# Performance work log

Hardware: AMD Instinct MI355X
Metric: run time of the kernel (lower is better)

The kernel has to match this reference:

```python
import jax, jax.numpy as jnp
import numpy as np

N_NODES = 50000
N_EDGES = 800000
N_GRAPHS = 64
NEG_SLOPE = 0.2


def _gat_layer(x, src, dst, W, a_src, a_dst, b, heads, out_ch):
    """PyG-style GATConv (concat=True, eval mode, self loops already in src/dst)."""
    N = x.shape[0]
    h = (x @ W).reshape(N, heads, out_ch)                 # [N,H,C]
    al_src = jnp.sum(h * a_src, axis=-1)                  # [N,H]
    al_dst = jnp.sum(h * a_dst, axis=-1)                  # [N,H]
    e = jax.nn.leaky_relu(al_src[src] + al_dst[dst], NEG_SLOPE)  # [E,H]
    m = jax.ops.segment_max(e, dst, num_segments=N)       # scatter-softmax (stable)
    e = jnp.exp(e - m[dst])
    s = jax.ops.segment_sum(e, dst, num_segments=N)
    alpha = e / (s[dst] + 1e-16)                          # [E,H]
    msg = h[src] * alpha[..., None]                       # [E,H,C]
    out = jax.ops.segment_sum(msg, dst, num_segments=N)   # [N,H,C]
    return out.reshape(N, heads * out_ch) + b


def setup_inputs() -> dict:
    key = jax.random.key(0)
    ks = jax.random.split(key, 20)
    x = jax.random.normal(ks[0], (N_NODES, 2), dtype=jnp.float32)
    edge_index = jax.random.randint(ks[1], (2, N_EDGES), 0, N_NODES, dtype=jnp.int64)
    batch = jnp.sort(jax.random.randint(ks[2], (N_NODES,), 0, N_GRAPHS, dtype=jnp.int64))

    def glorot(k, shape):
        fan = sum(shape)
        return jax.random.uniform(k, shape, jnp.float32, -1.0, 1.0) * jnp.sqrt(6.0 / fan)

    return {
        "x": x, "edge_index": edge_index, "batch": batch,
        # gat1: 2 -> 64, heads=2, concat -> 128
        "w1": glorot(ks[3], (2, 128)),
        "a_src1": glorot(ks[4], (2, 64)),
        "a_dst1": glorot(ks[5], (2, 64)),
        "b1": jnp.zeros((128,), jnp.float32),
        # gat2: 128 -> 64, heads=1
        "w2": glorot(ks[6], (128, 64)),
        "a_src2": glorot(ks[7], (1, 64)),
        "a_dst2": glorot(ks[8], (1, 64)),
        "b2": jnp.zeros((64,), jnp.float32),
        # gat3: 64 -> 64, heads=1
        "w3": glorot(ks[9], (64, 64)),
        "a_src3": glorot(ks[10], (1, 64)),
        "a_dst3": glorot(ks[11], (1, 64)),
        "b3": jnp.zeros((64,), jnp.float32),
        # MLP head
        "fw1": glorot(ks[12], (64, 32)),
        "fb1": jnp.zeros((32,), jnp.float32),
        "fw2": glorot(ks[13], (32, 1)),
        "fb2": jnp.zeros((1,), jnp.float32),
    }


def reference(x, edge_index, batch,
              w1, a_src1, a_dst1, b1,
              w2, a_src2, a_dst2, b2,
              w3, a_src3, a_dst3, b3,
              fw1, fb1, fw2, fb2):
    N = x.shape[0]
    loops = jnp.arange(N, dtype=edge_index.dtype)
    src = jnp.concatenate([edge_index[0], loops])  # add self loops (PyG default)
    dst = jnp.concatenate([edge_index[1], loops])

    h = jax.nn.elu(_gat_layer(x, src, dst, w1, a_src1, a_dst1, b1, heads=2, out_ch=64))
    h = jax.nn.elu(_gat_layer(h, src, dst, w2, a_src2, a_dst2, b2, heads=1, out_ch=64))
    h = jax.nn.elu(_gat_layer(h, src, dst, w3, a_src3, a_dst3, b3, heads=1, out_ch=64))

    # global mean pool
    sums = jax.ops.segment_sum(h, batch, num_segments=N_GRAPHS)          # [B,64]
    cnts = jax.ops.segment_sum(jnp.ones((N,), h.dtype), batch, num_segments=N_GRAPHS)
    g = sums / jnp.maximum(cnts, 1.0)[:, None]

    g = jax.nn.relu(g @ fw1 + fb1)
    return g @ fw2 + fb2
```

## Files before the change

kernel.cpp:

```cpp
#include <hip/hip_runtime.h>
#include <hip/hip_bf16.h>
#include <math.h>

#define NN 50000
#define NE 800000
#define ET 850000
#define NG 64

#define NBUK 125
#define BS   400
#define CHK  8192
#define NCH  104
#define NHIST (NBUK * NCH)
#define NSB  ((NHIST + 255) / 256)


__global__ __launch_bounds__(256) void hist_k(const int* __restrict__ ei,
                                              int* __restrict__ ghist) {
    __shared__ int h[NBUK];
    int c = blockIdx.x, t = threadIdx.x;
    for (int i = t; i < NBUK; i += 256) h[i] = 0;
    __syncthreads();
    int e0 = c * CHK;
    int e1 = min(ET, e0 + CHK);
    for (int e = e0 + t; e < e1; e += 256) {
        int dst = (e < NE) ? ei[NE + e] : (e - NE);
        atomicAdd(&h[dst / BS], 1);
    }
    __syncthreads();
    for (int b = t; b < NBUK; b += 256) ghist[b * NCH + c] = h[b];
}

__global__ __launch_bounds__(256) void gscan1_k(const int* __restrict__ in,
                                                int* __restrict__ out,
                                                int* __restrict__ bsum, int n) {
    int t = threadIdx.x;
    int idx = blockIdx.x * 256 + t;
    int v = (idx < n) ? in[idx] : 0;
    int lane = t & 63, wave = t >> 6;
    int inc = v;
#pragma unroll
    for (int d = 1; d < 64; d <<= 1) {
        int u = __shfl_up(inc, d);
        if (lane >= d) inc += u;
    }
    __shared__ int wtot[4];
    if (lane == 63) wtot[wave] = inc;
    __syncthreads();
    int wpre = 0;
    for (int w = 0; w < wave; w++) wpre += wtot[w];
    if (idx < n) out[idx] = wpre + inc - v;
    if (t == 255) bsum[blockIdx.x] = wpre + inc;
}

__global__ __launch_bounds__(256) void gscan2_k(const int* __restrict__ bsum,
                                                int* __restrict__ bpre, int nb,
                                                int* __restrict__ tailp, int tailv) {
    int t = threadIdx.x;
    int v = (t < nb) ? bsum[t] : 0;
    int lane = t & 63, wave = t >> 6;
    int inc = v;
#pragma unroll
    for (int d = 1; d < 64; d <<= 1) {
        int u = __shfl_up(inc, d);
        if (lane >= d) inc += u;
    }
    __shared__ int wtot[4];
    if (lane == 63) wtot[wave] = inc;
    __syncthreads();
    int wpre = 0;
    for (int w = 0; w < wave; w++) wpre += wtot[w];
    if (t < nb) bpre[t] = wpre + inc - v;
    if (t == 0 && tailp) *tailp = tailv;
}

__global__ __launch_bounds__(256) void gscan3_k(int* __restrict__ out,
                                                const int* __restrict__ bpre, int n) {
    int idx = blockIdx.x * 256 + threadIdx.x;
    if (idx < n) out[idx] += bpre[blockIdx.x];
}

__global__ __launch_bounds__(256) void part_k(const int* __restrict__ ei,
                                              const int* __restrict__ gbase,
                                              int* __restrict__ packed) {
    __shared__ int cur[NBUK];
    __shared__ int baseL[NBUK];
    int c = blockIdx.x, t = threadIdx.x;
    for (int i = t; i < NBUK; i += 256) {
        cur[i] = 0;
        baseL[i] = gbase[i * NCH + c];
    }
    __syncthreads();
    int e0 = c * CHK;
    int e1 = min(ET, e0 + CHK);
    for (int e = e0 + t; e < e1; e += 256) {
        int src, dst;
        if (e < NE) { src = ei[e]; dst = ei[NE + e]; }
        else        { src = dst = e - NE; }
        int b = dst / BS;
        int r = atomicAdd(&cur[b], 1);
        packed[baseL[b] + r] = ((dst - b * BS) << 17) | src;
    }
}

__global__ __launch_bounds__(256) void csr_k(const int* __restrict__ packed,
                                             const int* __restrict__ gbase,
                                             int* __restrict__ csr,
                                             int* __restrict__ offsets) {
    __shared__ int cnt[BS];
    __shared__ int sc[2][512];
    __shared__ int cur[BS];
    __shared__ int Ss, Ts;
    int b = blockIdx.x, t = threadIdx.x;
    for (int i = t; i < BS; i += 256) cnt[i] = 0;
    if (t == 0) {
        Ss = gbase[b * NCH];
        Ts = (b == NBUK - 1) ? ET : gbase[(b + 1) * NCH];
    }
    __syncthreads();
    int n0 = Ss, n1 = Ts;
    for (int i = n0 + t; i < n1; i += 256) {
        int p = packed[i];
        atomicAdd(&cnt[p >> 17], 1);
    }
    __syncthreads();
    for (int i = t; i < 512; i += 256) sc[0][i] = (i < BS) ? cnt[i] : 0;
    __syncthreads();
    int pp = 0;
    for (int d = 1; d < 512; d <<= 1) {
        for (int i = t; i < 512; i += 256) {
            int v = sc[pp][i];
            if (i >= d) v += sc[pp][i - d];
            sc[pp ^ 1][i] = v;
        }
        pp ^= 1;
        __syncthreads();
    }
    for (int i = t; i < BS; i += 256) {
        int pre = (i == 0) ? 0 : sc[pp][i - 1];
        offsets[b * BS + i] = Ss + pre;
        cur[i] = Ss + pre;
    }
    __syncthreads();
    for (int i = n0 + t; i < n1; i += 256) {
        int p = packed[i];
        int pos = atomicAdd(&cur[p >> 17], 1);
        csr[pos] = p & 0x1FFFF;
    }
}

__global__ __launch_bounds__(256) void sortw_k(const int* __restrict__ offsets,
                                               int* __restrict__ csr) {
    int gt = blockIdx.x * blockDim.x + threadIdx.x;
    int n = gt >> 6;
    int lane = gt & 63;
    if (n >= NN) return;
    int b0 = offsets[n], b1 = offsets[n + 1];
    int deg = b1 - b0;
    if (deg <= 1) return;
    if (deg <= 64) {
        int v = (lane < deg) ? csr[b0 + lane] : 0x7FFFFFFF;
#pragma unroll
        for (int k = 2; k <= 64; k <<= 1) {
#pragma unroll
            for (int j = k >> 1; j > 0; j >>= 1) {
                int partner = __shfl_xor(v, j);
                bool up = ((lane & k) == 0);
                bool keepmin = (((lane & j) == 0) == up);
                v = keepmin ? min(v, partner) : max(v, partner);
            }
        }
        if (lane < deg) csr[b0 + lane] = v;
    } else if (lane == 0) {
        for (int i = b0 + 1; i < b1; i++) {
            int v = csr[i];
            int j = i - 1;
            while (j >= b0 && csr[j] > v) { csr[j + 1] = csr[j]; j--; }
            csr[j + 1] = v;
        }
    }
}


__global__ __launch_bounds__(256) void feat1b_k(const float* __restrict__ x,
                                                const float* __restrict__ w1,
                                                const float* __restrict__ as1,
                                                const float* __restrict__ ad1,
                                                float* __restrict__ alS,
                                                float* __restrict__ alD) {
    int t = threadIdx.x;
    int tt = t & 127;
    int n = blockIdx.x * 2 + (t >> 7);
    float x0 = x[n * 2 + 0], x1 = x[n * 2 + 1];
    float v = x0 * w1[tt] + x1 * w1[128 + tt];
    int head = (t >> 6) & 1, lane = t & 63;
    float ps = v * as1[tt];
    float pd = v * ad1[tt];
    for (int d = 32; d; d >>= 1) {
        ps += __shfl_down(ps, d);
        pd += __shfl_down(pd, d);
    }
    if (lane == 0) {
        alS[n * 2 + head] = ps;
        alD[n * 2 + head] = pd;
    }
}


__global__ __launch_bounds__(256) void agg1_k(const float2* __restrict__ x2,
                                              const float* __restrict__ w1,
                                              const float* __restrict__ alS,
                                              const float* __restrict__ alD,
                                              const float* __restrict__ bias,
                                              const int* __restrict__ offsets,
                                              const int* __restrict__ csr,
                                              float* __restrict__ out) {
    __shared__ float4 wslds[4][64];
    int t = threadIdx.x;
    int wave = t >> 6, lane = t & 63, grp = lane >> 4, c4 = lane & 15;
    int gl = lane & 15;
    int n = blockIdx.x * 4 + wave;
    int b0 = offsets[n], b1 = offsets[n + 1];
    int deg = b1 - b0;
    float2 adv = ((const float2*)alD)[n];
    const float2* alS2 = (const float2*)alS;

    float4 wa0 = ((const float4*)w1)[c4];
    float4 wa1 = ((const float4*)w1)[16 + c4];
    float4 wb0 = ((const float4*)(w1 + 128))[c4];
    float4 wb1 = ((const float4*)(w1 + 128))[16 + c4];
    float4 acc0 = make_float4(0.f, 0.f, 0.f, 0.f);
    float4 acc1 = make_float4(0.f, 0.f, 0.f, 0.f);
    float inv0, inv1;

    if (deg <= 64) {
        bool valid = lane < deg;
        int s = 0; float ev0 = -1e30f, ev1 = -1e30f;
        float2 xs = make_float2(0.f, 0.f);
        if (valid) {
            s = csr[b0 + lane];
            float2 al = alS2[s];
            xs = x2[s];
            float e0 = al.x + adv.x;
            ev0 = e0 > 0.f ? e0 : 0.2f * e0;
            float e1 = al.y + adv.y;
            ev1 = e1 > 0.f ? e1 : 0.2f * e1;
        }
        float m0 = ev0, m1 = ev1;
#pragma unroll
        for (int d = 32; d; d >>= 1) {
            m0 = fmaxf(m0, __shfl_xor(m0, d));
            m1 = fmaxf(m1, __shfl_xor(m1, d));
        }
        if (valid) {
            float w0 = expf(ev0 - m0);
            float w1v = expf(ev1 - m1);
            wslds[wave][lane] = make_float4(w0, w1v, xs.x, xs.y);
        }
        float ssum0 = 0.f, ssum1 = 0.f;
#pragma unroll
        for (int k = 0; k < 4; k++) {
            int j = gl + 16 * k;
            if (j < deg) {
                float4 f = wslds[wave][j];
                ssum0 += f.x;
                ssum1 += f.y;
            }
        }
        for (int d = 8; d; d >>= 1) {
            ssum0 += __shfl_xor(ssum0, d);
            ssum1 += __shfl_xor(ssum1, d);
        }
        inv0 = 1.f / (ssum0 + 1e-16f);
        inv1 = 1.f / (ssum1 + 1e-16f);
        int j = grp;
        for (; j + 12 < deg; j += 16) {
            float4 f0 = wslds[wave][j];
            float4 f1 = wslds[wave][j + 4];
            float4 f2 = wslds[wave][j + 8];
            float4 f3 = wslds[wave][j + 12];
            float4 v;
            v.x = f0.z * wa0.x + f0.w * wb0.x;
            v.y = f0.z * wa0.y + f0.w * wb0.y;
            v.z = f0.z * wa0.z + f0.w * wb0.z;
            v.w = f0.z * wa0.w + f0.w * wb0.w;
            acc0.x = fmaf(f0.x, v.x, acc0.x);
            acc0.y = fmaf(f0.x, v.y, acc0.y);
            acc0.z = fmaf(f0.x, v.z, acc0.z);
            acc0.w = fmaf(f0.x, v.w, acc0.w);
            v.x = f0.z * wa1.x + f0.w * wb1.x;
            v.y = f0.z * wa1.y + f0.w * wb1.y;
            v.z = f0.z * wa1.z + f0.w * wb1.z;
            v.w = f0.z * wa1.w + f0.w * wb1.w;
            acc1.x = fmaf(f0.y, v.x, acc1.x);
            acc1.y = fmaf(f0.y, v.y, acc1.y);
            acc1.z = fmaf(f0.y, v.z, acc1.z);
            acc1.w = fmaf(f0.y, v.w, acc1.w);
            v.x = f1.z * wa0.x + f1.w * wb0.x;
            v.y = f1.z * wa0.y + f1.w * wb0.y;
            v.z = f1.z * wa0.z + f1.w * wb0.z;
            v.w = f1.z * wa0.w + f1.w * wb0.w;
            acc0.x = fmaf(f1.x, v.x, acc0.x);
            acc0.y = fmaf(f1.x, v.y, acc0.y);
            acc0.z = fmaf(f1.x, v.z, acc0.z);
            acc0.w = fmaf(f1.x, v.w, acc0.w);
            v.x = f1.z * wa1.x + f1.w * wb1.x;
            v.y = f1.z * wa1.y + f1.w * wb1.y;
            v.z = f1.z * wa1.z + f1.w * wb1.z;
            v.w = f1.z * wa1.w + f1.w * wb1.w;
            acc1.x = fmaf(f1.y, v.x, acc1.x);
            acc1.y = fmaf(f1.y, v.y, acc1.y);
            acc1.z = fmaf(f1.y, v.z, acc1.z);
            acc1.w = fmaf(f1.y, v.w, acc1.w);
            v.x = f2.z * wa0.x + f2.w * wb0.x;
            v.y = f2.z * wa0.y + f2.w * wb0.y;
            v.z = f2.z * wa0.z + f2.w * wb0.z;
            v.w = f2.z * wa0.w + f2.w * wb0.w;
            acc0.x = fmaf(f2.x, v.x, acc0.x);
            acc0.y = fmaf(f2.x, v.y, acc0.y);
            acc0.z = fmaf(f2.x, v.z, acc0.z);
            acc0.w = fmaf(f2.x, v.w, acc0.w);
            v.x = f2.z * wa1.x + f2.w * wb1.x;
            v.y = f2.z * wa1.y + f2.w * wb1.y;
            v.z = f2.z * wa1.z + f2.w * wb1.z;
            v.w = f2.z * wa1.w + f2.w * wb1.w;
            acc1.x = fmaf(f2.y, v.x, acc1.x);
            acc1.y = fmaf(f2.y, v.y, acc1.y);
            acc1.z = fmaf(f2.y, v.z, acc1.z);
            acc1.w = fmaf(f2.y, v.w, acc1.w);
            v.x = f3.z * wa0.x + f3.w * wb0.x;
            v.y = f3.z * wa0.y + f3.w * wb0.y;
            v.z = f3.z * wa0.z + f3.w * wb0.z;
            v.w = f3.z * wa0.w + f3.w * wb0.w;
            acc0.x = fmaf(f3.x, v.x, acc0.x);
            acc0.y = fmaf(f3.x, v.y, acc0.y);
            acc0.z = fmaf(f3.x, v.z, acc0.z);
            acc0.w = fmaf(f3.x, v.w, acc0.w);
            v.x = f3.z * wa1.x + f3.w * wb1.x;
            v.y = f3.z * wa1.y + f3.w * wb1.y;
            v.z = f3.z * wa1.z + f3.w * wb1.z;
            v.w = f3.z * wa1.w + f3.w * wb1.w;
            acc1.x = fmaf(f3.y, v.x, acc1.x);
            acc1.y = fmaf(f3.y, v.y, acc1.y);
            acc1.z = fmaf(f3.y, v.z, acc1.z);
            acc1.w = fmaf(f3.y, v.w, acc1.w);
        }
        for (; j < deg; j += 4) {
            float4 f0 = wslds[wave][j];
            float4 v;
            v.x = f0.z * wa0.x + f0.w * wb0.x;
            v.y = f0.z * wa0.y + f0.w * wb0.y;
            v.z = f0.z * wa0.z + f0.w * wb0.z;
            v.w = f0.z * wa0.w + f0.w * wb0.w;
            acc0.x = fmaf(f0.x, v.x, acc0.x);
            acc0.y = fmaf(f0.x, v.y, acc0.y);
            acc0.z = fmaf(f0.x, v.z, acc0.z);
            acc0.w = fmaf(f0.x, v.w, acc0.w);
            v.x = f0.z * wa1.x + f0.w * wb1.x;
            v.y = f0.z * wa1.y + f0.w * wb1.y;
            v.z = f0.z * wa1.z + f0.w * wb1.z;
            v.w = f0.z * wa1.w + f0.w * wb1.w;
            acc1.x = fmaf(f0.y, v.x, acc1.x);
            acc1.y = fmaf(f0.y, v.y, acc1.y);
            acc1.z = fmaf(f0.y, v.z, acc1.z);
            acc1.w = fmaf(f0.y, v.w, acc1.w);
        }
    } else {
        for (int head = 0; head < 2; head++) {
            float ad = head ? adv.y : adv.x;
            float4 wa = head ? wa1 : wa0, wb = head ? wb1 : wb0;
            float m = -1e30f;
            for (int i = b0 + gl; i < b1; i += 16) {
                int s = csr[i];
                float ev = alS[s * 2 + head] + ad;
                ev = ev > 0.f ? ev : 0.2f * ev;
                m = fmaxf(m, ev);
            }
            for (int d = 8; d; d >>= 1) m = fmaxf(m, __shfl_xor(m, d));
            float ssum = 0.f;
            for (int i = b0 + gl; i < b1; i += 16) {
                int s = csr[i];
                float ev = alS[s * 2 + head] + ad;
                ev = ev > 0.f ? ev : 0.2f * ev;
                float w = expf(ev - m);
                ssum += w;
            }
            for (int d = 8; d; d >>= 1) ssum += __shfl_xor(ssum, d);
            float invh = 1.f / (ssum + 1e-16f);
            float4 acc = make_float4(0.f, 0.f, 0.f, 0.f);
            for (int i = b0 + grp; i < b1; i += 4) {
                int s = csr[i];
                float ev = alS[s * 2 + head] + ad;
                ev = ev > 0.f ? ev : 0.2f * ev;
                float w = expf(ev - m);
                float2 xs = x2[s];
                float4 v;
                v.x = xs.x * wa.x + xs.y * wb.x;
                v.y = xs.x * wa.y + xs.y * wb.y;
                v.z = xs.x * wa.z + xs.y * wb.z;
                v.w = xs.x * wa.w + xs.y * wb.w;
                acc.x = fmaf(w, v.x, acc.x);
                acc.y = fmaf(w, v.y, acc.y);
                acc.z = fmaf(w, v.z, acc.z);
                acc.w = fmaf(w, v.w, acc.w);
            }
            if (head == 0) { acc0 = acc; inv0 = invh; }
            else           { acc1 = acc; inv1 = invh; }
        }
    }
#pragma unroll
    for (int mask = 16; mask <= 32; mask <<= 1) {
        acc0.x += __shfl_xor(acc0.x, mask);
        acc0.y += __shfl_xor(acc0.y, mask);
        acc0.z += __shfl_xor(acc0.z, mask);
        acc0.w += __shfl_xor(acc0.w, mask);
        acc1.x += __shfl_xor(acc1.x, mask);
        acc1.y += __shfl_xor(acc1.y, mask);
        acc1.z += __shfl_xor(acc1.z, mask);
        acc1.w += __shfl_xor(acc1.w, mask);
    }
    if (grp < 2) {
        float4 acc = (grp == 0) ? acc0 : acc1;
        float inv = (grp == 0) ? inv0 : inv1;
        float4 b = ((const float4*)bias)[grp * 16 + c4];
        float4 r;
        r.x = acc.x * inv + b.x;
        r.y = acc.y * inv + b.y;
        r.z = acc.z * inv + b.z;
        r.w = acc.w * inv + b.w;
        r.x = r.x > 0.f ? r.x : expm1f(r.x);
        r.y = r.y > 0.f ? r.y : expm1f(r.y);
        r.z = r.z > 0.f ? r.z : expm1f(r.z);
        r.w = r.w > 0.f ? r.w : expm1f(r.w);
        ((float4*)out)[((size_t)n * 2 + grp) * 16 + c4] = r;
    }
}


template <int K>
__global__ __launch_bounds__(256) void gemm_al_k(const float* __restrict__ in,
                                                 const float* __restrict__ W,
                                                 const float* __restrict__ as,
                                                 const float* __restrict__ ad,
                                                 float* __restrict__ h,
                                                 float* __restrict__ alS,
                                                 float* __restrict__ alD) {
    __shared__ float Wl[K * 64];
    __shared__ float rowb[16][K];
    int t = threadIdx.x;
    for (int i = t; i < K * 64; i += 256) Wl[i] = W[i];
    int wave = t >> 6, c = t & 63;
    int nb = blockIdx.x * 16 + wave * 4;
#pragma unroll
    for (int r = 0; r < 4; r++) {
        const float* row = in + (size_t)(nb + r) * K;
        for (int k = c; k < K; k += 64) rowb[wave * 4 + r][k] = row[k];
    }
    __syncthreads();
    const float* rb0 = rowb[wave * 4 + 0];
    const float* rb1 = rowb[wave * 4 + 1];
    const float* rb2 = rowb[wave * 4 + 2];
    const float* rb3 = rowb[wave * 4 + 3];
    float a0 = 0.f, a1 = 0.f, a2 = 0.f, a3 = 0.f;
#pragma unroll 4
    for (int k = 0; k < K; k++) {
        float wv = Wl[k * 64 + c];
        a0 = fmaf(rb0[k], wv, a0);
        a1 = fmaf(rb1[k], wv, a1);
        a2 = fmaf(rb2[k], wv, a2);
        a3 = fmaf(rb3[k], wv, a3);
    }
    h[(size_t)(nb + 0) * 64 + c] = a0;
    h[(size_t)(nb + 1) * 64 + c] = a1;
    h[(size_t)(nb + 2) * 64 + c] = a2;
    h[(size_t)(nb + 3) * 64 + c] = a3;
    float asc = as[c], adc = ad[c];
    float ps0 = a0 * asc, pd0 = a0 * adc;
    float ps1 = a1 * asc, pd1 = a1 * adc;
    float ps2 = a2 * asc, pd2 = a2 * adc;
    float ps3 = a3 * asc, pd3 = a3 * adc;
    for (int d = 32; d; d >>= 1) {
        ps0 += __shfl_down(ps0, d); pd0 += __shfl_down(pd0, d);
        ps1 += __shfl_down(ps1, d); pd1 += __shfl_down(pd1, d);
        ps2 += __shfl_down(ps2, d); pd2 += __shfl_down(pd2, d);
        ps3 += __shfl_down(ps3, d); pd3 += __shfl_down(pd3, d);
    }
    if (c == 0) {
        alS[nb + 0] = ps0; alD[nb + 0] = pd0;
        alS[nb + 1] = ps1; alD[nb + 1] = pd1;
        alS[nb + 2] = ps2; alD[nb + 2] = pd2;
        alS[nb + 3] = ps3; alD[nb + 3] = pd3;
    }
}


__global__ __launch_bounds__(256) void aggf2_k(const float4* __restrict__ h4,
                                               const float* __restrict__ alS,
                                               const float* __restrict__ alD,
                                               const float* __restrict__ bias,
                                               const int* __restrict__ offsets,
                                               const int* __restrict__ csr,
                                               float* __restrict__ out) {
    __shared__ float2 wlds[4][64];
    int t = threadIdx.x;
    int wave = t >> 6, lane = t & 63, grp = lane >> 4, c4 = lane & 15;
    int gl = lane & 15;
    int n = blockIdx.x * 4 + wave;
    int b0 = offsets[n], b1 = offsets[n + 1];
    int deg = b1 - b0;
    float adn = alD[n];

    float4 acc = make_float4(0.f, 0.f, 0.f, 0.f);
    float inv;

    if (deg <= 64) {
        bool valid = lane < deg;
        int s = 0; float ev = -1e30f;
        if (valid) {
            s = csr[b0 + lane];
            float e0 = alS[s] + adn;
            ev = e0 > 0.f ? e0 : 0.2f * e0;
        }
        float m = ev;
#pragma unroll
        for (int d = 32; d; d >>= 1) m = fmaxf(m, __shfl_xor(m, d));
        if (valid) {
            float w = expf(ev - m);
            wlds[wave][lane] = make_float2(w, __int_as_float(s));
        }
        float ssum = 0.f;
#pragma unroll
        for (int k = 0; k < 4; k++) {
            int j = gl + 16 * k;
            if (j < deg) ssum += wlds[wave][j].x;
        }
        for (int d = 8; d; d >>= 1) ssum += __shfl_xor(ssum, d);
        inv = 1.f / (ssum + 1e-16f);
        int j = grp;
        for (; j + 12 < deg; j += 16) {
            float2 f0 = wlds[wave][j];
            float2 f1 = wlds[wave][j + 4];
            float2 f2 = wlds[wave][j + 8];
            float2 f3 = wlds[wave][j + 12];
            float4 v0 = h4[(size_t)__float_as_int(f0.y) * 16 + c4];
            float4 v1 = h4[(size_t)__float_as_int(f1.y) * 16 + c4];
            float4 v2 = h4[(size_t)__float_as_int(f2.y) * 16 + c4];
            float4 v3 = h4[(size_t)__float_as_int(f3.y) * 16 + c4];
            acc.x = fmaf(f0.x, v0.x, acc.x);
            acc.y = fmaf(f0.x, v0.y, acc.y);
            acc.z = fmaf(f0.x, v0.z, acc.z);
            acc.w = fmaf(f0.x, v0.w, acc.w);
            acc.x = fmaf(f1.x, v1.x, acc.x);
            acc.y = fmaf(f1.x, v1.y, acc.y);
            acc.z = fmaf(f1.x, v1.z, acc.z);
            acc.w = fmaf(f1.x, v1.w, acc.w);
            acc.x = fmaf(f2.x, v2.x, acc.x);
            acc.y = fmaf(f2.x, v2.y, acc.y);
            acc.z = fmaf(f2.x, v2.z, acc.z);
            acc.w = fmaf(f2.x, v2.w, acc.w);
            acc.x = fmaf(f3.x, v3.x, acc.x);
            acc.y = fmaf(f3.x, v3.y, acc.y);
            acc.z = fmaf(f3.x, v3.z, acc.z);
            acc.w = fmaf(f3.x, v3.w, acc.w);
        }
        for (; j < deg; j += 4) {
            float2 f0 = wlds[wave][j];
            float4 v0 = h4[(size_t)__float_as_int(f0.y) * 16 + c4];
            acc.x = fmaf(f0.x, v0.x, acc.x);
            acc.y = fmaf(f0.x, v0.y, acc.y);
            acc.z = fmaf(f0.x, v0.z, acc.z);
            acc.w = fmaf(f0.x, v0.w, acc.w);
        }
    } else {
        float m = -1e30f;
        for (int i = b0 + gl; i < b1; i += 16) {
            int s = csr[i];
            float ev = alS[s] + adn;
            ev = ev > 0.f ? ev : 0.2f * ev;
            m = fmaxf(m, ev);
        }
        for (int d = 8; d; d >>= 1) m = fmaxf(m, __shfl_xor(m, d));
        float ssum = 0.f;
        for (int i = b0 + gl; i < b1; i += 16) {
            int s = csr[i];
            float ev = alS[s] + adn;
            ev = ev > 0.f ? ev : 0.2f * ev;
            float w = expf(ev - m);
            ssum += w;
        }
        for (int d = 8; d; d >>= 1) ssum += __shfl_xor(ssum, d);
        inv = 1.f / (ssum + 1e-16f);
        for (int i = b0 + grp; i < b1; i += 4) {
            int s = csr[i];
            float ev = alS[s] + adn;
            ev = ev > 0.f ? ev : 0.2f * ev;
            float w = expf(ev - m);
            float4 v = h4[(size_t)s * 16 + c4];
            acc.x = fmaf(w, v.x, acc.x);
            acc.y = fmaf(w, v.y, acc.y);
            acc.z = fmaf(w, v.z, acc.z);
            acc.w = fmaf(w, v.w, acc.w);
        }
    }
#pragma unroll
    for (int mask = 16; mask <= 32; mask <<= 1) {
        acc.x += __shfl_xor(acc.x, mask);
        acc.y += __shfl_xor(acc.y, mask);
        acc.z += __shfl_xor(acc.z, mask);
        acc.w += __shfl_xor(acc.w, mask);
    }
    if (grp == 0) {
        float4 b = ((const float4*)bias)[c4];
        float4 r;
        r.x = acc.x * inv + b.x;
        r.y = acc.y * inv + b.y;
        r.z = acc.z * inv + b.z;
        r.w = acc.w * inv + b.w;
        r.x = r.x > 0.f ? r.x : expm1f(r.x);
        r.y = r.y > 0.f ? r.y : expm1f(r.y);
        r.z = r.z > 0.f ? r.z : expm1f(r.z);
        r.w = r.w > 0.f ? r.w : expm1f(r.w);
        ((float4*)out)[(size_t)n * 16 + c4] = r;
    }
}


__global__ __launch_bounds__(1024) void pool_k(const float* __restrict__ h,
                                               const int* __restrict__ batch,
                                               float* __restrict__ gout) {
    int g = blockIdx.x;
    __shared__ int sb, se;
    __shared__ float partial[16][64];
    int t = threadIdx.x, wave = t >> 6, c = t & 63;
    if (t == 0) {
        int lo = 0, hi = NN;
        while (lo < hi) { int mid = (lo + hi) >> 1; if (batch[mid] < g) lo = mid + 1; else hi = mid; }
        sb = lo;
        lo = 0; hi = NN;
        while (lo < hi) { int mid = (lo + hi) >> 1; if (batch[mid] < g + 1) lo = mid + 1; else hi = mid; }
        se = lo;
    }
    __syncthreads();
    float acc = 0.f;
    for (int r = sb + wave; r < se; r += 16) acc += h[(size_t)r * 64 + c];
    partial[wave][c] = acc;
    __syncthreads();
    if (wave == 0) {
        float s = 0.f;
#pragma unroll
        for (int wv = 0; wv < 16; wv++) s += partial[wv][c];
        int cnt = se - sb;
        gout[g * 64 + c] = s / fmaxf((float)cnt, 1.0f);
    }
}


__global__ __launch_bounds__(64) void mlp_k(const float* __restrict__ g,
                                            const float* __restrict__ fw1,
                                            const float* __restrict__ fb1,
                                            const float* __restrict__ fw2,
                                            const float* __restrict__ fb2,
                                            float* __restrict__ out) {
    int gi = blockIdx.x;
    __shared__ float gv[64];
    __shared__ float hid[32];
    int t = threadIdx.x;
    gv[t] = g[gi * 64 + t];
    __syncthreads();
    if (t < 32) {
        float a = fb1[t];
        for (int c = 0; c < 64; c++) a += gv[c] * fw1[c * 32 + t];
        hid[t] = a > 0.f ? a : 0.f;
    }
    __syncthreads();
    if (t == 0) {
        float o = fb2[0];
        for (int j = 0; j < 32; j++) o += hid[j] * fw2[j];
        out[gi] = o;
    }
}


extern "C" void kernel_launch(void* const* d_in, const int* in_sizes, int n_in,
                              void* d_out, int out_size, void* d_ws, size_t ws_size,
                              hipStream_t stream) {
    const float* x   = (const float*)d_in[0];
    const int*   ei  = (const int*)d_in[1];
    const int*   bat = (const int*)d_in[2];
    const float* w1  = (const float*)d_in[3];
    const float* as1 = (const float*)d_in[4];
    const float* ad1 = (const float*)d_in[5];
    const float* b1  = (const float*)d_in[6];
    const float* w2  = (const float*)d_in[7];
    const float* as2 = (const float*)d_in[8];
    const float* ad2 = (const float*)d_in[9];
    const float* b2  = (const float*)d_in[10];
    const float* w3  = (const float*)d_in[11];
    const float* as3 = (const float*)d_in[12];
    const float* ad3 = (const float*)d_in[13];
    const float* b3  = (const float*)d_in[14];
    const float* fw1 = (const float*)d_in[15];
    const float* fb1 = (const float*)d_in[16];
    const float* fw2 = (const float*)d_in[17];
    const float* fb2 = (const float*)d_in[18];
    float* out = (float*)d_out;

    char* ws = (char*)d_ws;
    size_t o = 0;
    auto alloc = [&](size_t bytes) -> void* {
        void* p = ws + o;
        o += (bytes + 255) & ~(size_t)255;
        return p;
    };
    int*    offsets = (int*)alloc((NN + 1) * sizeof(int));
    int*    ghist   = (int*)alloc(NHIST * sizeof(int));
    int*    gbase   = (int*)alloc(NHIST * sizeof(int));
    int*    bsum    = (int*)alloc(NSB * sizeof(int));
    int*    bpre    = (int*)alloc(NSB * sizeof(int));
    int*    packed  = (int*)alloc(ET * sizeof(int));
    int*    csr     = (int*)alloc(ET * sizeof(int));
    float*  l1out   = (float*)alloc((size_t)NN * 128 * sizeof(float));
    float*  hX      = (float*)alloc((size_t)NN * 64 * sizeof(float));
    float*  l2out   = (float*)alloc((size_t)NN * 64 * sizeof(float));
    float*  l3out   = (float*)alloc((size_t)NN * 64 * sizeof(float));
    float*  alS     = (float*)alloc((size_t)NN * 2 * sizeof(float));
    float*  alD     = (float*)alloc((size_t)NN * 2 * sizeof(float));
    float*  gbuf    = (float*)alloc((size_t)NG * 64 * sizeof(float));

    hist_k<<<NCH, 256, 0, stream>>>(ei, ghist);
    gscan1_k<<<NSB, 256, 0, stream>>>(ghist, gbase, bsum, NHIST);
    gscan2_k<<<1, 256, 0, stream>>>(bsum, bpre, NSB, offsets + NN, ET);
    gscan3_k<<<NSB, 256, 0, stream>>>(gbase, bpre, NHIST);
    part_k<<<NCH, 256, 0, stream>>>(ei, gbase, packed);
    csr_k<<<NBUK, 256, 0, stream>>>(packed, gbase, csr, offsets);
    sortw_k<<<NN / 4, 256, 0, stream>>>(offsets, csr);

    feat1b_k<<<NN / 2, 256, 0, stream>>>(x, w1, as1, ad1, alS, alD);
    agg1_k<<<NN / 4, 256, 0, stream>>>((const float2*)x, w1, alS, alD, b1, offsets, csr, l1out);

    gemm_al_k<128><<<NN / 16, 256, 0, stream>>>(l1out, w2, as2, ad2, hX, alS, alD);
    aggf2_k<<<NN / 4, 256, 0, stream>>>((const float4*)hX, alS, alD, b2, offsets, csr, l2out);

    gemm_al_k<64><<<NN / 16, 256, 0, stream>>>(l2out, w3, as3, ad3, hX, alS, alD);
    aggf2_k<<<NN / 4, 256, 0, stream>>>((const float4*)hX, alS, alD, b3, offsets, csr, l3out);

    pool_k<<<NG, 1024, 0, stream>>>(l3out, bat, gbuf);
    mlp_k<<<NG, 64, 0, stream>>>(gbuf, fw1, fb1, fw2, fb2, out);
}
```

Measured before the change: 281.9 us.

## Process four nodes per wave in aggregation kernels and fold scan fixup into consumers

The aggregation kernels now give each wave four destination nodes instead of one. When all four degrees are at most 64, their gathers, softmax reductions and shuffles are interleaved so more memory requests are in flight at once and weight and bias loads are shared; otherwise they fall back to a per-node helper. Separately, the gscan3 fixup kernel is removed and its block prefix is added on the fly in part_k and csr_k, saving one launch and one pass over the histogram. The interleaved path raises register and LDS use per wave, which may lower occupancy, and the grid shrinks to a quarter as many blocks.

Result: no change. 285.1 us (+1.1%).

```diff
diff --git a/kernel.cpp b/kernel.cpp
--- a/kernel.cpp
+++ b/kernel.cpp
@@ -74,21 +74,17 @@
     if (t == 0 && tailp) *tailp = tailv;
 }
 
-__global__ __launch_bounds__(256) void gscan3_k(int* __restrict__ out,
-                                                const int* __restrict__ bpre, int n) {
-    int idx = blockIdx.x * 256 + threadIdx.x;
-    if (idx < n) out[idx] += bpre[blockIdx.x];
-}
-
 __global__ __launch_bounds__(256) void part_k(const int* __restrict__ ei,
                                               const int* __restrict__ gbase,
+                                              const int* __restrict__ bpre,
                                               int* __restrict__ packed) {
     __shared__ int cur[NBUK];
     __shared__ int baseL[NBUK];
     int c = blockIdx.x, t = threadIdx.x;
     for (int i = t; i < NBUK; i += 256) {
+        int idx = i * NCH + c;
         cur[i] = 0;
-        baseL[i] = gbase[i * NCH + c];
+        baseL[i] = gbase[idx] + bpre[idx >> 8];
     }
     __syncthreads();
     int e0 = c * CHK;
@@ -105,6 +101,7 @@
 
 __global__ __launch_bounds__(256) void csr_k(const int* __restrict__ packed,
                                              const int* __restrict__ gbase,
+                                             const int* __restrict__ bpre,
                                              int* __restrict__ csr,
                                              int* __restrict__ offsets) {
     __shared__ int cnt[BS];
@@ -114,8 +111,10 @@
     int b = blockIdx.x, t = threadIdx.x;
     for (int i = t; i < BS; i += 256) cnt[i] = 0;
     if (t == 0) {
-        Ss = gbase[b * NCH];
-        Ts = (b == NBUK - 1) ? ET : gbase[(b + 1) * NCH];
+        int i0 = b * NCH;
+        Ss = gbase[i0] + bpre[i0 >> 8];
+        int i1 = (b + 1) * NCH;
+        Ts = (b == NBUK - 1) ? ET : (gbase[i1] + bpre[i1 >> 8]);
     }
     __syncthreads();
     int n0 = Ss, n1 = Ts;
@@ -207,28 +206,17 @@
 }
 
 
-__global__ __launch_bounds__(256) void agg1_k(const float2* __restrict__ x2,
-                                              const float* __restrict__ w1,
-                                              const float* __restrict__ alS,
-                                              const float* __restrict__ alD,
-                                              const float* __restrict__ bias,
-                                              const int* __restrict__ offsets,
-                                              const int* __restrict__ csr,
-                                              float* __restrict__ out) {
-    __shared__ float4 wslds[4][64];
-    int t = threadIdx.x;
-    int wave = t >> 6, lane = t & 63, grp = lane >> 4, c4 = lane & 15;
-    int gl = lane & 15;
-    int n = blockIdx.x * 4 + wave;
+__device__ __forceinline__ void agg1_node_single(
+        int n, const float2* __restrict__ x2, const float* __restrict__ alS,
+        const float* __restrict__ alD, const int* __restrict__ offsets,
+        const int* __restrict__ csr, float4* __restrict__ slot,
+        const float4 wa0, const float4 wa1, const float4 wb0, const float4 wb1,
+        const float4 bsel, float* __restrict__ out,
+        int lane, int grp, int c4, int gl) {
     int b0 = offsets[n], b1 = offsets[n + 1];
     int deg = b1 - b0;
     float2 adv = ((const float2*)alD)[n];
     const float2* alS2 = (const float2*)alS;
-
-    float4 wa0 = ((const float4*)w1)[c4];
-    float4 wa1 = ((const float4*)w1)[16 + c4];
-    float4 wb0 = ((const float4*)(w1 + 128))[c4];
-    float4 wb1 = ((const float4*)(w1 + 128))[16 + c4];
     float4 acc0 = make_float4(0.f, 0.f, 0.f, 0.f);
     float4 acc1 = make_float4(0.f, 0.f, 0.f, 0.f);
     float inv0, inv1;
@@ -255,14 +243,14 @@
         if (valid) {
             float w0 = expf(ev0 - m0);
             float w1v = expf(ev1 - m1);
-            wslds[wave][lane] = make_float4(w0, w1v, xs.x, xs.y);
+            slot[lane] = make_float4(w0, w1v, xs.x, xs.y);
         }
         float ssum0 = 0.f, ssum1 = 0.f;
 #pragma unroll
         for (int k = 0; k < 4; k++) {
             int j = gl + 16 * k;
             if (j < deg) {
-                float4 f = wslds[wave][j];
+                float4 f = slot[j];
                 ssum0 += f.x;
                 ssum1 += f.y;
             }
@@ -273,80 +261,8 @@
         }
         inv0 = 1.f / (ssum0 + 1e-16f);
         inv1 = 1.f / (ssum1 + 1e-16f);
-        int j = grp;
-        for (; j + 12 < deg; j += 16) {
-            float4 f0 = wslds[wave][j];
-            float4 f1 = wslds[wave][j + 4];
-            float4 f2 = wslds[wave][j + 8];
-            float4 f3 = wslds[wave][j + 12];
-            float4 v;
-            v.x = f0.z * wa0.x + f0.w * wb0.x;
-            v.y = f0.z * wa0.y + f0.w * wb0.y;
-            v.z = f0.z * wa0.z + f0.w * wb0.z;
-            v.w = f0.z * wa0.w + f0.w * wb0.w;
-            acc0.x = fmaf(f0.x, v.x, acc0.x);
-            acc0.y = fmaf(f0.x, v.y, acc0.y);
-            acc0.z = fmaf(f0.x, v.z, acc0.z);
-            acc0.w = fmaf(f0.x, v.w, acc0.w);
-            v.x = f0.z * wa1.x + f0.w * wb1.x;
-            v.y = f0.z * wa1.y + f0.w * wb1.y;
-            v.z = f0.z * wa1.z + f0.w * wb1.z;
-            v.w = f0.z * wa1.w + f0.w * wb1.w;
-            acc1.x = fmaf(f0.y, v.x, acc1.x);
-            acc1.y = fmaf(f0.y, v.y, acc1.y);
-            acc1.z = fmaf(f0.y, v.z, acc1.z);
-            acc1.w = fmaf(f0.y, v.w, acc1.w);
-            v.x = f1.z * wa0.x + f1.w * wb0.x;
-            v.y = f1.z * wa0.y + f1.w * wb0.y;
-            v.z = f1.z * wa0.z + f1.w * wb0.z;
-            v.w = f1.z * wa0.w + f1.w * wb0.w;
-            acc0.x = fmaf(f1.x, v.x, acc0.x);
-            acc0.y = fmaf(f1.x, v.y, acc0.y);
-            acc0.z = fmaf(f1.x, v.z, acc0.z);
-            acc0.w = fmaf(f1.x, v.w, acc0.w);
-            v.x = f1.z * wa1.x + f1.w * wb1.x;
-            v.y = f1.z * wa1.y + f1.w * wb1.y;
-            v.z = f1.z * wa1.z + f1.w * wb1.z;
-            v.w = f1.z * wa1.w + f1.w * wb1.w;
-            acc1.x = fmaf(f1.y, v.x, acc1.x);
-            acc1.y = fmaf(f1.y, v.y, acc1.y);
-            acc1.z = fmaf(f1.y, v.z, acc1.z);
-            acc1.w = fmaf(f1.y, v.w, acc1.w);
-            v.x = f2.z * wa0.x + f2.w * wb0.x;
-            v.y = f2.z * wa0.y + f2.w * wb0.y;
-            v.z = f2.z * wa0.z + f2.w * wb0.z;
-            v.w = f2.z * wa0.w + f2.w * wb0.w;
-            acc0.x = fmaf(f2.x, v.x, acc0.x);
-            acc0.y = fmaf(f2.x, v.y, acc0.y);
-            acc0.z = fmaf(f2.x, v.z, acc0.z);
-            acc0.w = fmaf(f2.x, v.w, acc0.w);
-            v.x = f2.z * wa1.x + f2.w * wb1.x;
-            v.y = f2.z * wa1.y + f2.w * wb1.y;
-            v.z = f2.z * wa1.z + f2.w * wb1.z;
-            v.w = f2.z * wa1.w + f2.w * wb1.w;
-            acc1.x = fmaf(f2.y, v.x, acc1.x);
-            acc1.y = fmaf(f2.y, v.y, acc1.y);
-            acc1.z = fmaf(f2.y, v.z, acc1.z);
-            acc1.w = fmaf(f2.y, v.w, acc1.w);
-            v.x = f3.z * wa0.x + f3.w * wb0.x;
-            v.y = f3.z * wa0.y + f3.w * wb0.y;
-            v.z = f3.z * wa0.z + f3.w * wb0.z;
-            v.w = f3.z * wa0.w + f3.w * wb0.w;
-            acc0.x = fmaf(f3.x, v.x, acc0.x);
-            acc0.y = fmaf(f3.x, v.y, acc0.y);
-            acc0.z = fmaf(f3.x, v.z, acc0.z);
-            acc0.w = fmaf(f3.x, v.w, acc0.w);
-            v.x = f3.z * wa1.x + f3.w * wb1.x;
-            v.y = f3.z * wa1.y + f3.w * wb1.y;
-            v.z = f3.z * wa1.z + f3.w * wb1.z;
-            v.w = f3.z * wa1.w + f3.w * wb1.w;
-            acc1.x = fmaf(f3.y, v.x, acc1.x);
-            acc1.y = fmaf(f3.y, v.y, acc1.y);
-            acc1.z = fmaf(f3.y, v.z, acc1.z);
-            acc1.w = fmaf(f3.y, v.w, acc1.w);
-        }
-        for (; j < deg; j += 4) {
-            float4 f0 = wslds[wave][j];
+        for (int j = grp; j < deg; j += 4) {
+            float4 f0 = slot[j];
             float4 v;
             v.x = f0.z * wa0.x + f0.w * wb0.x;
             v.y = f0.z * wa0.y + f0.w * wb0.y;
@@ -422,17 +338,250 @@
     if (grp < 2) {
         float4 acc = (grp == 0) ? acc0 : acc1;
         float inv = (grp == 0) ? inv0 : inv1;
-        float4 b = ((const float4*)bias)[grp * 16 + c4];
         float4 r;
-        r.x = acc.x * inv + b.x;
-        r.y = acc.y * inv + b.y;
-        r.z = acc.z * inv + b.z;
-        r.w = acc.w * inv + b.w;
+        r.x = acc.x * inv + bsel.x;
+        r.y = acc.y * inv + bsel.y;
+        r.z = acc.z * inv + bsel.z;
+        r.w = acc.w * inv + bsel.w;
         r.x = r.x > 0.f ? r.x : expm1f(r.x);
         r.y = r.y > 0.f ? r.y : expm1f(r.y);
         r.z = r.z > 0.f ? r.z : expm1f(r.z);
         r.w = r.w > 0.f ? r.w : expm1f(r.w);
         ((float4*)out)[((size_t)n * 2 + grp) * 16 + c4] = r;
+    }
+}
+
+
+__global__ __launch_bounds__(256) void agg1_k(const float2* __restrict__ x2,
+                                              const float* __restrict__ w1,
+                                              const float* __restrict__ alS,
+                                              const float* __restrict__ alD,
+                                              const float* __restrict__ bias,
+                                              const int* __restrict__ offsets,
+                                              const int* __restrict__ csr,
+                                              float* __restrict__ out) {
+    __shared__ float4 wslds[4][4][64];
+    int t = threadIdx.x;
+    int wave = t >> 6, lane = t & 63, grp = lane >> 4, c4 = lane & 15;
+    int gl = lane & 15;
+    int nb = blockIdx.x * 16 + wave * 4;
+    const float2* alS2 = (const float2*)alS;
+
+    float4 wa0 = ((const float4*)w1)[c4];
+    float4 wa1 = ((const float4*)w1)[16 + c4];
+    float4 wb0 = ((const float4*)(w1 + 128))[c4];
+    float4 wb1 = ((const float4*)(w1 + 128))[16 + c4];
+    float4 bsel = (grp < 2) ? ((const float4*)bias)[grp * 16 + c4]
+                            : make_float4(0.f, 0.f, 0.f, 0.f);
+
+    int b0[4], deg[4];
+#pragma unroll
+    for (int k = 0; k < 4; k++) {
+        b0[k] = offsets[nb + k];
+        deg[k] = offsets[nb + k + 1] - b0[k];
+    }
+    bool allsmall = deg[0] <= 64 && deg[1] <= 64 && deg[2] <= 64 && deg[3] <= 64;
+
+    if (allsmall) {
+        int sv[4];
+        float2 alv[4], xsv[4];
+        float2 adv[4];
+#pragma unroll
+        for (int k = 0; k < 4; k++) adv[k] = ((const float2*)alD)[nb + k];
+#pragma unroll
+        for (int k = 0; k < 4; k++) {
+            sv[k] = 0;
+            if (lane < deg[k]) sv[k] = csr[b0[k] + lane];
+        }
+#pragma unroll
+        for (int k = 0; k < 4; k++) {
+            alv[k] = make_float2(0.f, 0.f);
+            xsv[k] = make_float2(0.f, 0.f);
+            if (lane < deg[k]) {
+                alv[k] = alS2[sv[k]];
+                xsv[k] = x2[sv[k]];
+            }
+        }
+        float ev0[4], ev1[4], m0[4], m1[4];
+#pragma unroll
+        for (int k = 0; k < 4; k++) {
+            ev0[k] = -1e30f; ev1[k] = -1e30f;
+            if (lane < deg[k]) {
+                float e0 = alv[k].x + adv[k].x;
+                ev0[k] = e0 > 0.f ? e0 : 0.2f * e0;
+                float e1 = alv[k].y + adv[k].y;
+                ev1[k] = e1 > 0.f ? e1 : 0.2f * e1;
+            }
+            m0[k] = ev0[k]; m1[k] = ev1[k];
+        }
+#pragma unroll
+        for (int d = 32; d; d >>= 1) {
+#pragma unroll
+            for (int k = 0; k < 4; k++) {
+                m0[k] = fmaxf(m0[k], __shfl_xor(m0[k], d));
+                m1[k] = fmaxf(m1[k], __shfl_xor(m1[k], d));
+            }
+        }
+#pragma unroll
+        for (int k = 0; k < 4; k++) {
+            if (lane < deg[k]) {
+                float w0 = expf(ev0[k] - m0[k]);
+                float w1v = expf(ev1[k] - m1[k]);
+                wslds[wave][k][lane] = make_float4(w0, w1v, xsv[k].x, xsv[k].y);
+            }
+        }
+        float ssum0[4] = {0.f, 0.f, 0.f, 0.f};
+        float ssum1[4] = {0.f, 0.f, 0.f, 0.f};
+#pragma unroll
+        for (int q = 0; q < 4; q++) {
+            int j = gl + 16 * q;
+#pragma unroll
+            for (int k = 0; k < 4; k++) {
+                if (j < deg[k]) {
+                    float4 f = wslds[wave][k][j];
+                    ssum0[k] += f.x;
+                    ssum1[k] += f.y;
+                }
+            }
+        }
+#pragma unroll
+        for (int d = 8; d; d >>= 1) {
+#pragma unroll
+            for (int k = 0; k < 4; k++) {
+                ssum0[k] += __shfl_xor(ssum0[k], d);
+                ssum1[k] += __shfl_xor(ssum1[k], d);
+            }
+        }
+#pragma unroll
+        for (int k = 0; k < 4; k++) {
+            float inv0 = 1.f / (ssum0[k] + 1e-16f);
+            float inv1 = 1.f / (ssum1[k] + 1e-16f);
+            float4 acc0 = make_float4(0.f, 0.f, 0.f, 0.f);
+            float4 acc1 = make_float4(0.f, 0.f, 0.f, 0.f);
+            const float4* slot = wslds[wave][k];
+            int dg = deg[k];
+            int j = grp;
+            for (; j + 12 < dg; j += 16) {
+                float4 f0 = slot[j];
+                float4 f1 = slot[j + 4];
+                float4 f2 = slot[j + 8];
+                float4 f3 = slot[j + 12];
+                float4 v;
+                v.x = f0.z * wa0.x + f0.w * wb0.x;
+                v.y = f0.z * wa0.y + f0.w * wb0.y;
+                v.z = f0.z * wa0.z + f0.w * wb0.z;
+                v.w = f0.z * wa0.w + f0.w * wb0.w;
+                acc0.x = fmaf(f0.x, v.x, acc0.x);
+                acc0.y = fmaf(f0.x, v.y, acc0.y);
+                acc0.z = fmaf(f0.x, v.z, acc0.z);
+                acc0.w = fmaf(f0.x, v.w, acc0.w);
+                v.x = f0.z * wa1.x + f0.w * wb1.x;
+                v.y = f0.z * wa1.y + f0.w * wb1.y;
+                v.z = f0.z * wa1.z + f0.w * wb1.z;
+                v.w = f0.z * wa1.w + f0.w * wb1.w;
+                acc1.x = fmaf(f0.y, v.x, acc1.x);
+                acc1.y = fmaf(f0.y, v.y, acc1.y);
+                acc1.z = fmaf(f0.y, v.z, acc1.z);
+                acc1.w = fmaf(f0.y, v.w, acc1.w);
+                v.x = f1.z * wa0.x + f1.w * wb0.x;
+                v.y = f1.z * wa0.y + f1.w * wb0.y;
+                v.z = f1.z * wa0.z + f1.w * wb0.z;
+                v.w = f1.z * wa0.w + f1.w * wb0.w;
+                acc0.x = fmaf(f1.x, v.x, acc0.x);
+                acc0.y = fmaf(f1.x, v.y, acc0.y);
+                acc0.z = fmaf(f1.x, v.z, acc0.z);
+                acc0.w = fmaf(f1.x, v.w, acc0.w);
+                v.x = f1.z * wa1.x + f1.w * wb1.x;
+                v.y = f1.z * wa1.y + f1.w * wb1.y;
+                v.z = f1.z * wa1.z + f1.w * wb1.z;
+                v.w = f1.z * wa1.w + f1.w * wb1.w;
+                acc1.x = fmaf(f1.y, v.x, acc1.x);
+                acc1.y = fmaf(f1.y, v.y, acc1.y);
+                acc1.z = fmaf(f1.y, v.z, acc1.z);
+                acc1.w = fmaf(f1.y, v.w, acc1.w);
+                v.x = f2.z * wa0.x + f2.w * wb0.x;
+                v.y = f2.z * wa0.y + f2.w * wb0.y;
+                v.z = f2.z * wa0.z + f2.w * wb0.z;
+                v.w = f2.z * wa0.w + f2.w * wb0.w;
+                acc0.x = fmaf(f2.x, v.x, acc0.x);
+                acc0.y = fmaf(f2.x, v.y, acc0.y);
+                acc0.z = fmaf(f2.x, v.z, acc0.z);
+                acc0.w = fmaf(f2.x, v.w, acc0.w);
+                v.x = f2.z * wa1.x + f2.w * wb1.x;
+                v.y = f2.z * wa1.y + f2.w * wb1.y;
+                v.z = f2.z * wa1.z + f2.w * wb1.z;
+                v.w = f2.z * wa1.w + f2.w * wb1.w;
+                acc1.x = fmaf(f2.y, v.x, acc1.x);
+                acc1.y = fmaf(f2.y, v.y, acc1.y);
+                acc1.z = fmaf(f2.y, v.z, acc1.z);
+                acc1.w = fmaf(f2.y, v.w, acc1.w);
+                v.x = f3.z * wa0.x + f3.w * wb0.x;
+                v.y = f3.z * wa0.y + f3.w * wb0.y;
+                v.z = f3.z * wa0.z + f3.w * wb0.z;
+                v.w = f3.z * wa0.w + f3.w * wb0.w;
+                acc0.x = fmaf(f3.x, v.x, acc0.x);
+                acc0.y = fmaf(f3.x, v.y, acc0.y);
+                acc0.z = fmaf(f3.x, v.z, acc0.z);
+                acc0.w = fmaf(f3.x, v.w, acc0.w);
+                v.x = f3.z * wa1.x + f3.w * wb1.x;
+                v.y = f3.z * wa1.y + f3.w * wb1.y;
+                v.z = f3.z * wa1.z + f3.w * wb1.z;
+                v.w = f3.z * wa1.w + f3.w * wb1.w;
+                acc1.x = fmaf(f3.y, v.x, acc1.x);
+                acc1.y = fmaf(f3.y, v.y, acc1.y);
+                acc1.z = fmaf(f3.y, v.z, acc1.z);
+                acc1.w = fmaf(f3.y, v.w, acc1.w);
+            }
+            for (; j < dg; j += 4) {
+                float4 f0 = slot[j];
+                float4 v;
+                v.x = f0.z * wa0.x + f0.w * wb0.x;
+                v.y = f0.z * wa0.y + f0.w * wb0.y;
+                v.z = f0.z * wa0.z + f0.w * wb0.z;
+                v.w = f0.z * wa0.w + f0.w * wb0.w;
+                acc0.x = fmaf(f0.x, v.x, acc0.x);
+                acc0.y = fmaf(f0.x, v.y, acc0.y);
+                acc0.z = fmaf(f0.x, v.z, acc0.z);
+                acc0.w = fmaf(f0.x, v.w, acc0.w);
+                v.x = f0.z * wa1.x + f0.w * wb1.x;
+                v.y = f0.z * wa1.y + f0.w * wb1.y;
+                v.z = f0.z * wa1.z + f0.w * wb1.z;
+                v.w = f0.z * wa1.w + f0.w * wb1.w;
+                acc1.x = fmaf(f0.y, v.x, acc1.x);
+                acc1.y = fmaf(f0.y, v.y, acc1.y);
+                acc1.z = fmaf(f0.y, v.z, acc1.z);
+                acc1.w = fmaf(f0.y, v.w, acc1.w);
+            }
+#pragma unroll
+            for (int mask = 16; mask <= 32; mask <<= 1) {
+                acc0.x += __shfl_xor(acc0.x, mask);
+                acc0.y += __shfl_xor(acc0.y, mask);
+                acc0.z += __shfl_xor(acc0.z, mask);
+                acc0.w += __shfl_xor(acc0.w, mask);
+                acc1.x += __shfl_xor(acc1.x, mask);
+                acc1.y += __shfl_xor(acc1.y, mask);
+                acc1.z += __shfl_xor(acc1.z, mask);
+                acc1.w += __shfl_xor(acc1.w, mask);
+            }
+            if (grp < 2) {
+                float4 acc = (grp == 0) ? acc0 : acc1;
+                float inv = (grp == 0) ? inv0 : inv1;
+                float4 r;
+                r.x = acc.x * inv + bsel.x;
+                r.y = acc.y * inv + bsel.y;
+                r.z = acc.z * inv + bsel.z;
+                r.w = acc.w * inv + bsel.w;
+                r.x = r.x > 0.f ? r.x : expm1f(r.x);
+                r.y = r.y > 0.f ? r.y : expm1f(r.y);
+                r.z = r.z > 0.f ? r.z : expm1f(r.z);
+                r.w = r.w > 0.f ? r.w : expm1f(r.w);
+                ((float4*)out)[((size_t)(nb + k) * 2 + grp) * 16 + c4] = r;
+            }
+        }
+    } else {
+        for (int k = 0; k < 4; k++)
+            agg1_node_single(nb + k, x2, alS, alD, offsets, csr, wslds[wave][k],
+                             wa0, wa1, wb0, wb1, bsel, out, lane, grp, c4, gl);
     }
 }
 
@@ -494,22 +643,15 @@
 }
 
 
-__global__ __launch_bounds__(256) void aggf2_k(const float4* __restrict__ h4,
-                                               const float* __restrict__ alS,
-                                               const float* __restrict__ alD,
-                                               const float* __restrict__ bias,
-                                               const int* __restrict__ offsets,
-                                               const int* __restrict__ csr,
-                                               float* __restrict__ out) {
-    __shared__ float2 wlds[4][64];
-    int t = threadIdx.x;
-    int wave = t >> 6, lane = t & 63, grp = lane >> 4, c4 = lane & 15;
-    int gl = lane & 15;
-    int n = blockIdx.x * 4 + wave;
+__device__ __forceinline__ void aggf2_node_single(
+        int n, const float4* __restrict__ h4, const float* __restrict__ alS,
+        const float* __restrict__ alD, const int* __restrict__ offsets,
+        const int* __restrict__ csr, float2* __restrict__ slot,
+        const float4 bsel, float* __restrict__ out,
+        int lane, int grp, int c4, int gl) {
     int b0 = offsets[n], b1 = offsets[n + 1];
     int deg = b1 - b0;
     float adn = alD[n];
-
     float4 acc = make_float4(0.f, 0.f, 0.f, 0.f);
     float inv;
 
@@ -526,22 +668,22 @@
         for (int d = 32; d; d >>= 1) m = fmaxf(m, __shfl_xor(m, d));
         if (valid) {
             float w = expf(ev - m);
-            wlds[wave][lane] = make_float2(w, __int_as_float(s));
+            slot[lane] = make_float2(w, __int_as_float(s));
         }
         float ssum = 0.f;
 #pragma unroll
         for (int k = 0; k < 4; k++) {
             int j = gl + 16 * k;
-            if (j < deg) ssum += wlds[wave][j].x;
+            if (j < deg) ssum += slot[j].x;
         }
         for (int d = 8; d; d >>= 1) ssum += __shfl_xor(ssum, d);
         inv = 1.f / (ssum + 1e-16f);
         int j = grp;
         for (; j + 12 < deg; j += 16) {
-            float2 f0 = wlds[wave][j];
-            float2 f1 = wlds[wave][j + 4];
-            float2 f2 = wlds[wave][j + 8];
-            float2 f3 = wlds[wave][j + 12];
+            float2 f0 = slot[j];
+            float2 f1 = slot[j + 4];
+            float2 f2 = slot[j + 8];
+            float2 f3 = slot[j + 12];
             float4 v0 = h4[(size_t)__float_as_int(f0.y) * 16 + c4];
             float4 v1 = h4[(size_t)__float_as_int(f1.y) * 16 + c4];
             float4 v2 = h4[(size_t)__float_as_int(f2.y) * 16 + c4];
@@ -564,7 +706,7 @@
             acc.w = fmaf(f3.x, v3.w, acc.w);
         }
         for (; j < deg; j += 4) {
-            float2 f0 = wlds[wave][j];
+            float2 f0 = slot[j];
             float4 v0 = h4[(size_t)__float_as_int(f0.y) * 16 + c4];
             acc.x = fmaf(f0.x, v0.x, acc.x);
             acc.y = fmaf(f0.x, v0.y, acc.y);
@@ -610,17 +752,158 @@
         acc.w += __shfl_xor(acc.w, mask);
     }
     if (grp == 0) {
-        float4 b = ((const float4*)bias)[c4];
         float4 r;
-        r.x = acc.x * inv + b.x;
-        r.y = acc.y * inv + b.y;
-        r.z = acc.z * inv + b.z;
-        r.w = acc.w * inv + b.w;
+        r.x = acc.x * inv + bsel.x;
+        r.y = acc.y * inv + bsel.y;
+        r.z = acc.z * inv + bsel.z;
+        r.w = acc.w * inv + bsel.w;
         r.x = r.x > 0.f ? r.x : expm1f(r.x);
         r.y = r.y > 0.f ? r.y : expm1f(r.y);
         r.z = r.z > 0.f ? r.z : expm1f(r.z);
         r.w = r.w > 0.f ? r.w : expm1f(r.w);
         ((float4*)out)[(size_t)n * 16 + c4] = r;
+    }
+}
+
+
+__global__ __launch_bounds__(256) void aggf2_k(const float4* __restrict__ h4,
+                                               const float* __restrict__ alS,
+                                               const float* __restrict__ alD,
+                                               const float* __restrict__ bias,
+                                               const int* __restrict__ offsets,
+                                               const int* __restrict__ csr,
+                                               float* __restrict__ out) {
+    __shared__ float2 wlds[4][4][64];
+    int t = threadIdx.x;
+    int wave = t >> 6, lane = t & 63, grp = lane >> 4, c4 = lane & 15;
+    int gl = lane & 15;
+    int nb = blockIdx.x * 16 + wave * 4;
+    float4 bsel = ((const float4*)bias)[c4];
+
+    int b0[4], deg[4];
+#pragma unroll
+    for (int k = 0; k < 4; k++) {
+        b0[k] = offsets[nb + k];
+        deg[k] = offsets[nb + k + 1] - b0[k];
+    }
+    bool allsmall = deg[0] <= 64 && deg[1] <= 64 && deg[2] <= 64 && deg[3] <= 64;
+
+    if (allsmall) {
+        int sv[4];
+        float alv[4], adv[4];
+#pragma unroll
+        for (int k = 0; k < 4; k++) adv[k] = alD[nb + k];
+#pragma unroll
+        for (int k = 0; k < 4; k++) {
+            sv[k] = 0;
+            if (lane < deg[k]) sv[k] = csr[b0[k] + lane];
+        }
+#pragma unroll
+        for (int k = 0; k < 4; k++) {
+            alv[k] = 0.f;
+            if (lane < deg[k]) alv[k] = alS[sv[k]];
+        }
+        float ev[4], m[4];
+#pragma unroll
+        for (int k = 0; k < 4; k++) {
+            ev[k] = -1e30f;
+            if (lane < deg[k]) {
+                float e0 = alv[k] + adv[k];
+                ev[k] = e0 > 0.f ? e0 : 0.2f * e0;
+            }
+            m[k] = ev[k];
+        }
+#pragma unroll
+        for (int d = 32; d; d >>= 1) {
+#pragma unroll
+            for (int k = 0; k < 4; k++) m[k] = fmaxf(m[k], __shfl_xor(m[k], d));
+        }
+#pragma unroll
+        for (int k = 0; k < 4; k++) {
+            if (lane < deg[k]) {
+                float w = expf(ev[k] - m[k]);
+                wlds[wave][k][lane] = make_float2(w, __int_as_float(sv[k]));
+            }
+        }
+        float ssum[4] = {0.f, 0.f, 0.f, 0.f};
+#pragma unroll
+        for (int q = 0; q < 4; q++) {
+            int j = gl + 16 * q;
+#pragma unroll
+            for (int k = 0; k < 4; k++) {
+                if (j < deg[k]) ssum[k] += wlds[wave][k][j].x;
+            }
+        }
+#pragma unroll
+        for (int d = 8; d; d >>= 1) {
+#pragma unroll
+            for (int k = 0; k < 4; k++) ssum[k] += __shfl_xor(ssum[k], d);
+        }
+#pragma unroll
+        for (int k = 0; k < 4; k++) {
+            float inv = 1.f / (ssum[k] + 1e-16f);
+            float4 acc = make_float4(0.f, 0.f, 0.f, 0.f);
+            const float2* slot = wlds[wave][k];
+            int dg = deg[k];
+            int j = grp;
+            for (; j + 12 < dg; j += 16) {
+                float2 f0 = slot[j];
+                float2 f1 = slot[j + 4];
+                float2 f2 = slot[j + 8];
+                float2 f3 = slot[j + 12];
+                float4 v0 = h4[(size_t)__float_as_int(f0.y) * 16 + c4];
+                float4 v1 = h4[(size_t)__float_as_int(f1.y) * 16 + c4];
+                float4 v2 = h4[(size_t)__float_as_int(f2.y) * 16 + c4];
+                float4 v3 = h4[(size_t)__float_as_int(f3.y) * 16 + c4];
+                acc.x = fmaf(f0.x, v0.x, acc.x);
+                acc.y = fmaf(f0.x, v0.y, acc.y);
+                acc.z = fmaf(f0.x, v0.z, acc.z);
+                acc.w = fmaf(f0.x, v0.w, acc.w);
+                acc.x = fmaf(f1.x, v1.x, acc.x);
+                acc.y = fmaf(f1.x, v1.y, acc.y);
+                acc.z = fmaf(f1.x, v1.z, acc.z);
+                acc.w = fmaf(f1.x, v1.w, acc.w);
+                acc.x = fmaf(f2.x, v2.x, acc.x);
+                acc.y = fmaf(f2.x, v2.y, acc.y);
+                acc.z = fmaf(f2.x, v2.z, acc.z);
+                acc.w = fmaf(f2.x, v2.w, acc.w);
+                acc.x = fmaf(f3.x, v3.x, acc.x);
+                acc.y = fmaf(f3.x, v3.y, acc.y);
+                acc.z = fmaf(f3.x, v3.z, acc.z);
+                acc.w = fmaf(f3.x, v3.w, acc.w);
+            }
+            for (; j < dg; j += 4) {
+                float2 f0 = slot[j];
+                float4 v0 = h4[(size_t)__float_as_int(f0.y) * 16 + c4];
+                acc.x = fmaf(f0.x, v0.x, acc.x);
+                acc.y = fmaf(f0.x, v0.y, acc.y);
+                acc.z = fmaf(f0.x, v0.z, acc.z);
+                acc.w = fmaf(f0.x, v0.w, acc.w);
+            }
+#pragma unroll
+            for (int mask = 16; mask <= 32; mask <<= 1) {
+                acc.x += __shfl_xor(acc.x, mask);
+                acc.y += __shfl_xor(acc.y, mask);
+                acc.z += __shfl_xor(acc.z, mask);
+                acc.w += __shfl_xor(acc.w, mask);
+            }
+            if (grp == 0) {
+                float4 r;
+                r.x = acc.x * inv + bsel.x;
+                r.y = acc.y * inv + bsel.y;
+                r.z = acc.z * inv + bsel.z;
+                r.w = acc.w * inv + bsel.w;
+                r.x = r.x > 0.f ? r.x : expm1f(r.x);
+                r.y = r.y > 0.f ? r.y : expm1f(r.y);
+                r.z = r.z > 0.f ? r.z : expm1f(r.z);
+                r.w = r.w > 0.f ? r.w : expm1f(r.w);
+                ((float4*)out)[(size_t)(nb + k) * 16 + c4] = r;
+            }
+        }
+    } else {
+        for (int k = 0; k < 4; k++)
+            aggf2_node_single(nb + k, h4, alS, alD, offsets, csr, wlds[wave][k],
+                              bsel, out, lane, grp, c4, gl);
     }
 }
 
@@ -730,19 +1013,18 @@
     hist_k<<<NCH, 256, 0, stream>>>(ei, ghist);
     gscan1_k<<<NSB, 256, 0, stream>>>(ghist, gbase, bsum, NHIST);
     gscan2_k<<<1, 256, 0, stream>>>(bsum, bpre, NSB, offsets + NN, ET);
-    gscan3_k<<<NSB, 256, 0, stream>>>(gbase, bpre, NHIST);
-    part_k<<<NCH, 256, 0, stream>>>(ei, gbase, packed);
-    csr_k<<<NBUK, 256, 0, stream>>>(packed, gbase, csr, offsets);
+    part_k<<<NCH, 256, 0, stream>>>(ei, gbase, bpre, packed);
+    csr_k<<<NBUK, 256, 0, stream>>>(packed, gbase, bpre, csr, offsets);
     sortw_k<<<NN / 4, 256, 0, stream>>>(offsets, csr);
 
     feat1b_k<<<NN / 2, 256, 0, stream>>>(x, w1, as1, ad1, alS, alD);
-    agg1_k<<<NN / 4, 256, 0, stream>>>((const float2*)x, w1, alS, alD, b1, offsets, csr, l1out);
+    agg1_k<<<NN / 16, 256, 0, stream>>>((const float2*)x, w1, alS, alD, b1, offsets, csr, l1out);
 
     gemm_al_k<128><<<NN / 16, 256, 0, stream>>>(l1out, w2, as2, ad2, hX, alS, alD);
-    aggf2_k<<<NN / 4, 256, 0, stream>>>((const float4*)hX, alS, alD, b2, offsets, csr, l2out);
+    aggf2_k<<<NN / 16, 256, 0, stream>>>((const float4*)hX, alS, alD, b2, offsets, csr, l2out);
 
     gemm_al_k<64><<<NN / 16, 256, 0, stream>>>(l2out, w3, as3, ad3, hX, alS, alD);
-    aggf2_k<<<NN / 4, 256, 0, stream>>>((const float4*)hX, alS, alD, b3, offsets, csr, l3out);
+    aggf2_k<<<NN / 16, 256, 0, stream>>>((const float4*)hX, alS, alD, b3, offsets, csr, l3out);
 
     pool_k<<<NG, 1024, 0, stream>>>(l3out, bat, gbuf);
     mlp_k<<<NG, 64, 0, stream>>>(gbuf, fw1, fb1, fw2, fb2, out);
```
